# Optimization experiments

Hardware: AMD Instinct MI355X
Metric: run time of the kernel (lower is better)

## Reference

```python
import jax, jax.numpy as jnp
import numpy as np

N_NODES = 100000
N_EDGES = 1600000
IN_DIM = 128
OUT_DIM = 64


def setup_inputs() -> dict:
    key = jax.random.key(0)
    k1, k2, k3, k4, k5, k6 = jax.random.split(key, 6)
    x = jax.random.normal(k1, (N_NODES, IN_DIM), dtype=jnp.float32)
    edge_row = jax.random.randint(k2, (N_EDGES,), 0, N_NODES, dtype=jnp.int32)
    edge_col = jax.random.randint(k3, (N_EDGES,), 0, N_NODES, dtype=jnp.int32)
    edge_val = jax.random.uniform(k4, (N_EDGES,), dtype=jnp.float32)
    W = jax.random.normal(k5, (IN_DIM, OUT_DIM), dtype=jnp.float32) * (1.0 / np.sqrt(IN_DIM))
    b = jax.random.normal(k6, (OUT_DIM,), dtype=jnp.float32) * 0.01
    return {"x": x, "edge_row": edge_row, "edge_col": edge_col,
            "edge_val": edge_val, "W": W, "b": b}


def reference(x, edge_row, edge_col, edge_val, W, b):
    # xw = Linear(x)  -> [N, OUT_DIM]
    xw = x @ W + b
    # SpMM: (A_hat @ xw)[r] = sum_e val[e] * xw[col[e]] for edges with row[e]==r
    msgs = edge_val[:, None] * xw[edge_col]          # [E, OUT_DIM]
    ax = jax.ops.segment_sum(msgs, edge_row, num_segments=N_NODES)  # [N, OUT_DIM]
    # ReLU; dropout p=0.0 is identity (eval mode)
    return jax.nn.relu(ax)
```

## Files before the change

kernel.cpp:

```cpp
#include <hip/hip_runtime.h>
#include <hip/hip_fp16.h>
#include <limits.h>

#define IN_DIM 128
#define OUT_DIM 64
#define NBUCK 782
#define RPB 128
#define CHUNK 4096
#define SCAP 4096


typedef _Float16 half8_t __attribute__((ext_vector_type(8)));
typedef float    f32x4  __attribute__((ext_vector_type(4)));

__device__ __forceinline__ int kmap(int g, int j) {
    return g * 4 + (j & 3) + 16 * (j >> 2);
}

__global__ __launch_bounds__(256) void wfrag_kernel(
    const float* __restrict__ W, __half* __restrict__ wf) {
    for (int idx = threadIdx.x; idx < 4 * 4 * 64 * 8; idx += 256) {
        const int j    = idx & 7;
        const int lane = (idx >> 3) & 63;
        const int ks   = (idx >> 9) & 3;
        const int n    = idx >> 11;
        const int col  = n * 16 + (lane & 15);
        const int k    = ks * 32 + kmap(lane >> 4, j);
        wf[idx] = __float2half(W[k * OUT_DIM + col]);
    }
}

__global__ __launch_bounds__(256) void gemm_mfma_kernel(
    const float* __restrict__ x, const __half* __restrict__ wf,
    const float* __restrict__ b, __half* __restrict__ xw, int n_nodes) {
    const int t  = threadIdx.x;
    const int l  = t & 63;
    const int wv = t >> 6;
    const int g  = l >> 4;
    const int rowbase = blockIdx.x * 64 + wv * 16;
    const int row = rowbase + (l & 15);
    const bool rok = row < n_nodes;
    const float* xr = x + (size_t)row * IN_DIM;

    half8_t bf[4][4];
    const half8_t* wf8 = (const half8_t*)wf;
    #pragma unroll
    for (int n = 0; n < 4; ++n)
        #pragma unroll
        for (int ks = 0; ks < 4; ++ks)
            bf[n][ks] = wf8[(n * 4 + ks) * 64 + l];

    half8_t af[4];
    #pragma unroll
    for (int ks = 0; ks < 4; ++ks) {
        float4 c0 = rok ? *(const float4*)(xr + ks * 32 + g * 4)
                        : make_float4(0.f, 0.f, 0.f, 0.f);
        float4 c1 = rok ? *(const float4*)(xr + ks * 32 + 16 + g * 4)
                        : make_float4(0.f, 0.f, 0.f, 0.f);
        half8_t a;
        a[0] = (_Float16)c0.x; a[1] = (_Float16)c0.y;
        a[2] = (_Float16)c0.z; a[3] = (_Float16)c0.w;
        a[4] = (_Float16)c1.x; a[5] = (_Float16)c1.y;
        a[6] = (_Float16)c1.z; a[7] = (_Float16)c1.w;
        af[ks] = a;
    }

    f32x4 acc[4];
    #pragma unroll
    for (int n = 0; n < 4; ++n) acc[n] = (f32x4){0.f, 0.f, 0.f, 0.f};

    #pragma unroll
    for (int ks = 0; ks < 4; ++ks)
        #pragma unroll
        for (int n = 0; n < 4; ++n)
            acc[n] = __builtin_amdgcn_mfma_f32_16x16x32_f16(af[ks], bf[n][ks], acc[n], 0, 0, 0);

    float bias[4];
    #pragma unroll
    for (int n = 0; n < 4; ++n) bias[n] = b[n * 16 + (l & 15)];

    #pragma unroll
    for (int n = 0; n < 4; ++n)
        #pragma unroll
        for (int q = 0; q < 4; ++q) {
            const int ro = rowbase + g * 4 + q;
            if (ro < n_nodes)
                xw[(size_t)ro * OUT_DIM + n * 16 + (l & 15)] =
                    __float2half(acc[n][q] + bias[n]);
        }
}

__global__ __launch_bounds__(256) void bucket_hist_kernel(
    const int* __restrict__ erow, int* __restrict__ bcount, int n_edges) {
    __shared__ int h[NBUCK];
    for (int i = threadIdx.x; i < NBUCK; i += 256) h[i] = 0;
    __syncthreads();
    const int stride = gridDim.x * blockDim.x;
    for (int e = blockIdx.x * blockDim.x + threadIdx.x; e < n_edges; e += stride)
        atomicAdd(&h[erow[e] >> 7], 1);
    __syncthreads();
    for (int i = threadIdx.x; i < NBUCK; i += 256)
        if (h[i]) atomicAdd(&bcount[i], h[i]);
}

__global__ __launch_bounds__(512) void bucket_scan_kernel(
    const int* __restrict__ bcount, int* __restrict__ bbase,
    int* __restrict__ cursor, int* __restrict__ row_ptr, int n_nodes) {
    const int t = threadIdx.x;
    const int i0 = 2 * t, i1 = 2 * t + 1;
    int v0 = (i0 < NBUCK) ? bcount[i0] : 0;
    int v1 = (i1 < NBUCK) ? bcount[i1] : 0;
    const int s = v0 + v1;
    int inc = s;
    #pragma unroll
    for (int d = 1; d < 64; d <<= 1) {
        int u = __shfl_up(inc, d, 64);
        if ((t & 63) >= d) inc += u;
    }
    __shared__ int wsum[8];
    if ((t & 63) == 63) wsum[t >> 6] = inc;
    __syncthreads();
    int wp = 0;
    #pragma unroll
    for (int w = 0; w < 8; ++w) if (w < (t >> 6)) wp += wsum[w];
    const int ex = wp + (inc - s);
    if (i0 < NBUCK) { bbase[i0] = ex;      cursor[i0] = ex; }
    if (i1 < NBUCK) { bbase[i1] = ex + v0; cursor[i1] = ex + v0; }
    if (t == 511) {
        bbase[NBUCK] = wp + inc;
        row_ptr[n_nodes] = wp + inc;
    }
}

__global__ __launch_bounds__(512) void partition_kernel(
    const int* __restrict__ erow, const int* __restrict__ ecol,
    const float* __restrict__ eval_, int* __restrict__ cursor,
    int2* __restrict__ ecs, int n_edges) {
    __shared__ int  hist[NBUCK];
    __shared__ int  lbase[NBUCK];
    __shared__ int  gdelta[NBUCK];
    __shared__ int2 data[CHUNK];
    __shared__ int  gpos[CHUNK];
    __shared__ int  wsum[8];

    const int t = threadIdx.x;
    const int base = blockIdx.x * CHUNK;
    const int cnt = min(CHUNK, n_edges - base);

    for (int i = t; i < NBUCK; i += 512) hist[i] = 0;
    __syncthreads();

    int   myrow[CHUNK / 512];
    int   mycol[CHUNK / 512];
    float myval[CHUNK / 512];
    #pragma unroll
    for (int i = 0; i < CHUNK / 512; ++i) {
        const int idx = t + i * 512;
        if (idx < cnt) {
            const int e = base + idx;
            myrow[i] = erow[e];
            mycol[i] = ecol[e];
            myval[i] = eval_[e];
            atomicAdd(&hist[myrow[i] >> 7], 1);
        }
    }
    __syncthreads();

    {
        const int i0 = 2 * t, i1 = 2 * t + 1;
        const int v0 = (i0 < NBUCK) ? hist[i0] : 0;
        const int v1 = (i1 < NBUCK) ? hist[i1] : 0;
        const int s = v0 + v1;
        int inc = s;
        #pragma unroll
        for (int d = 1; d < 64; d <<= 1) {
            int u = __shfl_up(inc, d, 64);
            if ((t & 63) >= d) inc += u;
        }
        if ((t & 63) == 63) wsum[t >> 6] = inc;
        __syncthreads();
        int wp = 0;
        #pragma unroll
        for (int w = 0; w < 8; ++w) if (w < (t >> 6)) wp += wsum[w];
        const int ex = wp + (inc - s);
        if (i0 < NBUCK) lbase[i0] = ex;
        if (i1 < NBUCK) lbase[i1] = ex + v0;
    }
    __syncthreads();

    for (int i = t; i < NBUCK; i += 512) {
        const int c = hist[i];
        gdelta[i] = c ? (atomicAdd(&cursor[i], c) - lbase[i]) : 0;
    }
    __syncthreads();

    #pragma unroll
    for (int i = 0; i < CHUNK / 512; ++i) {
        const int idx = t + i * 512;
        if (idx < cnt) {
            const int bk = myrow[i] >> 7;
            const int slot = atomicAdd(&lbase[bk], 1);
            int2 p;
            p.x = (int)(((unsigned)(myrow[i] & (RPB - 1)) << 25) |
                        ((unsigned)mycol[i] << 7));
            p.y = __float_as_int(myval[i]);
            data[slot] = p;
            gpos[slot] = slot + gdelta[bk];
        }
    }
    __syncthreads();

    for (int slot = t; slot < cnt; slot += 512)
        ecs[gpos[slot]] = data[slot];
}

__global__ __launch_bounds__(256) void sort_bucket_kernel(
    const int* __restrict__ bbase, int2* __restrict__ ecs,
    int* __restrict__ row_ptr, int n_nodes) {
    __shared__ int2 data[SCAP];
    __shared__ int2 data2[SCAP];
    __shared__ int  hist[RPB];
    __shared__ int  wtot;

    const int bk = blockIdx.x;
    const int t  = threadIdx.x;
    const int s  = bbase[bk];
    const int e  = bbase[bk + 1];
    const int cnt = e - s;
    const int rbase = bk * RPB;

    if (cnt > SCAP) {
        for (int r = t; r < RPB; r += 256)
            if (rbase + r < n_nodes) row_ptr[rbase + r] = INT_MIN;
        return;
    }

    for (int i = t; i < RPB; i += 256) hist[i] = 0;
    __syncthreads();

    for (int i = t; i < cnt; i += 256) {
        const int2 p = ecs[s + i];
        data[i] = p;
        atomicAdd(&hist[((unsigned)p.x) >> 25], 1);
    }
    __syncthreads();

    int inc = 0, v = 0;
    if (t < RPB) {
        v = hist[t];
        inc = v;
        #pragma unroll
        for (int d = 1; d < 64; d <<= 1) {
            int u = __shfl_up(inc, d, 64);
            if ((t & 63) >= d) inc += u;
        }
        if (t == 63) wtot = inc;
    }
    __syncthreads();
    if (t < RPB) {
        if (t >= 64) inc += wtot;
        const int ex = inc - v;
        if (rbase + t < n_nodes) row_ptr[rbase + t] = s + ex;
        hist[t] = ex;
    }
    __syncthreads();

    for (int i = t; i < cnt; i += 256) {
        const int2 p = data[i];
        const int r = (int)(((unsigned)p.x) >> 25);
        const int pos = atomicAdd(&hist[r], 1);
        data2[pos] = p;
    }
    __syncthreads();

    for (int i = t; i < cnt; i += 256) ecs[s + i] = data2[i];
}

__global__ __launch_bounds__(256) void gather_relu_kernel(
    const __half* __restrict__ xw, const int2* __restrict__ ecs,
    const int* __restrict__ row_ptr, const int* __restrict__ bbase,
    float* __restrict__ out, int n_nodes, int n_edges) {
    const int lane = threadIdx.x & 63;
    const int q    = lane & 7;
    const int g    = lane >> 3;
    const int wid  = (blockIdx.x * blockDim.x + threadIdx.x) >> 6;
    const int r0   = wid * 2;
    const int r1   = r0 + 1;
    if (r0 >= n_nodes) return;
    const bool has1 = (r1 < n_nodes);
    const char* xwb = (const char*)xw;

    const int s0raw = row_ptr[r0];
    const int s1raw = has1 ? row_ptr[r1] : INT_MIN;
    const bool ok0 = (s0raw != INT_MIN);
    const bool ok1 = has1 && (s1raw != INT_MIN);

    float acc0[8], acc1[8];
    #pragma unroll
    for (int i = 0; i < 8; ++i) { acc0[i] = 0.f; acc1[i] = 0.f; }

    if (ok0 && (ok1 || !has1)) {
        int e0;
        {
            const int n0 = row_ptr[r0 + 1];
            e0 = (n0 == INT_MIN) ? bbase[(r0 >> 7) + 1] : n0;
        }
        int e1 = 0, j1 = 0;
        if (ok1) {
            const int n1 = row_ptr[r1 + 1];
            e1 = (n1 == INT_MIN) ? bbase[(r1 >> 7) + 1] : n1;
            j1 = s1raw;
        }
        int j0 = s0raw;

        while (j0 < e0 || j1 < e1) {
            const bool a0 = j0 < e0;
            const bool a1 = j1 < e1;
            int2 p0, p1; float v0 = 0.f, v1 = 0.f;
            unsigned off0 = 0, off1 = 0;
            if (a0) {
                const int ei = j0 + g;
                p0 = ecs[min(ei, n_edges - 1)];
                v0 = (ei < e0) ? __int_as_float(p0.y) : 0.f;
                off0 = (((unsigned)p0.x) & 0x01FFFF80u) | ((unsigned)q << 4);
            }
            if (a1) {
                const int ei = j1 + g;
                p1 = ecs[min(ei, n_edges - 1)];
                v1 = (ei < e1) ? __int_as_float(p1.y) : 0.f;
                off1 = (((unsigned)p1.x) & 0x01FFFF80u) | ((unsigned)q << 4);
            }
            union { uint4 u; __half2 h[4]; } U0, U1;
            if (a0) U0.u = *(const uint4*)(xwb + off0);
            if (a1) U1.u = *(const uint4*)(xwb + off1);
            if (a0) {
                #pragma unroll
                for (int i = 0; i < 4; ++i) {
                    const float2 f = __half22float2(U0.h[i]);
                    acc0[2 * i]     = fmaf(v0, f.x, acc0[2 * i]);
                    acc0[2 * i + 1] = fmaf(v0, f.y, acc0[2 * i + 1]);
                }
                j0 += 8;
            }
            if (a1) {
                #pragma unroll
                for (int i = 0; i < 4; ++i) {
                    const float2 f = __half22float2(U1.h[i]);
                    acc1[2 * i]     = fmaf(v1, f.x, acc1[2 * i]);
                    acc1[2 * i + 1] = fmaf(v1, f.y, acc1[2 * i + 1]);
                }
                j1 += 8;
            }
        }
    } else {
        #pragma unroll 1
        for (int rr = 0; rr < 2; ++rr) {
            const int r = r0 + rr;
            if (r >= n_nodes) break;
            float* acc = rr ? acc1 : acc0;
            const int sr = row_ptr[r];
            if (sr != INT_MIN) {
                int er;
                const int nr = row_ptr[r + 1];
                er = (nr == INT_MIN) ? bbase[(r >> 7) + 1] : nr;
                for (int j = sr; j < er; j += 8) {
                    const int ei = j + g;
                    const int2 p = ecs[min(ei, n_edges - 1)];
                    const float v = (ei < er) ? __int_as_float(p.y) : 0.f;
                    const unsigned off = (((unsigned)p.x) & 0x01FFFF80u) | ((unsigned)q << 4);
                    union { uint4 u; __half2 h[4]; } U;
                    U.u = *(const uint4*)(xwb + off);
                    #pragma unroll
                    for (int i = 0; i < 4; ++i) {
                        const float2 f = __half22float2(U.h[i]);
                        acc[2 * i]     = fmaf(v, f.x, acc[2 * i]);
                        acc[2 * i + 1] = fmaf(v, f.y, acc[2 * i + 1]);
                    }
                }
            } else {
                const int bk = r >> 7;
                const int bs = bbase[bk], be = bbase[bk + 1];
                const unsigned rl = (unsigned)(r & (RPB - 1));
                for (int j = bs; j < be; ++j) {
                    const int2 p = ecs[j];
                    if ((((unsigned)p.x) >> 25) == rl) {
                        const float v = __int_as_float(p.y);
                        const unsigned off = (((unsigned)p.x) & 0x01FFFF80u) | ((unsigned)q << 4);
                        union { uint4 u; __half2 h[4]; } U;
                        U.u = *(const uint4*)(xwb + off);
                        #pragma unroll
                        for (int i = 0; i < 4; ++i) {
                            const float2 f = __half22float2(U.h[i]);
                            acc[2 * i]     = fmaf(v * 0.125f, f.x, acc[2 * i]);
                            acc[2 * i + 1] = fmaf(v * 0.125f, f.y, acc[2 * i + 1]);
                        }
                    }
                }
                #pragma unroll
                for (int i = 0; i < 8; ++i) acc[i] *= 1.0f;
            }
        }
    }

    #pragma unroll
    for (int d = 8; d < 64; d <<= 1) {
        #pragma unroll
        for (int i = 0; i < 8; ++i) {
            acc0[i] += __shfl_xor(acc0[i], d, 64);
            acc1[i] += __shfl_xor(acc1[i], d, 64);
        }
    }

    if (g == 0) {
        {
            float4 o0, o1;
            o0.x = fmaxf(acc0[0], 0.f); o0.y = fmaxf(acc0[1], 0.f);
            o0.z = fmaxf(acc0[2], 0.f); o0.w = fmaxf(acc0[3], 0.f);
            o1.x = fmaxf(acc0[4], 0.f); o1.y = fmaxf(acc0[5], 0.f);
            o1.z = fmaxf(acc0[6], 0.f); o1.w = fmaxf(acc0[7], 0.f);
            float* op = out + (size_t)r0 * OUT_DIM + q * 8;
            *(float4*)(op)     = o0;
            *(float4*)(op + 4) = o1;
        }
        if (has1) {
            float4 o0, o1;
            o0.x = fmaxf(acc1[0], 0.f); o0.y = fmaxf(acc1[1], 0.f);
            o0.z = fmaxf(acc1[2], 0.f); o0.w = fmaxf(acc1[3], 0.f);
            o1.x = fmaxf(acc1[4], 0.f); o1.y = fmaxf(acc1[5], 0.f);
            o1.z = fmaxf(acc1[6], 0.f); o1.w = fmaxf(acc1[7], 0.f);
            float* op = out + (size_t)r1 * OUT_DIM + q * 8;
            *(float4*)(op)     = o0;
            *(float4*)(op + 4) = o1;
        }
    }
}

__global__ __launch_bounds__(256) void edge_scatter_kernel(
    const __half* __restrict__ xw, const int* __restrict__ erow,
    const int* __restrict__ ecol, const float* __restrict__ eval_,
    float* __restrict__ out, int n_edges) {
    const int lane  = threadIdx.x & 63;
    const int wid   = (blockIdx.x * blockDim.x + threadIdx.x) >> 6;
    const int nwave = (gridDim.x * blockDim.x) >> 6;
    for (int e = wid; e < n_edges; e += nwave) {
        const float m = eval_[e] * __half2float(xw[(size_t)ecol[e] * OUT_DIM + lane]);
        atomicAdd(&out[(size_t)erow[e] * OUT_DIM + lane], m);
    }
}

__global__ __launch_bounds__(256) void relu_kernel(float4* __restrict__ p, int n4) {
    const int stride = gridDim.x * blockDim.x;
    for (int i = blockIdx.x * blockDim.x + threadIdx.x; i < n4; i += stride) {
        float4 v = p[i];
        v.x = fmaxf(v.x, 0.f); v.y = fmaxf(v.y, 0.f);
        v.z = fmaxf(v.z, 0.f); v.w = fmaxf(v.w, 0.f);
        p[i] = v;
    }
}

extern "C" void kernel_launch(void* const* d_in, const int* in_sizes, int n_in,
                              void* d_out, int out_size, void* d_ws, size_t ws_size,
                              hipStream_t stream) {
    const float* x     = (const float*)d_in[0];
    const int*   erow  = (const int*)d_in[1];
    const int*   ecol  = (const int*)d_in[2];
    const float* eval_ = (const float*)d_in[3];
    const float* W     = (const float*)d_in[4];
    const float* b     = (const float*)d_in[5];
    float*       out   = (float*)d_out;

    const int n_nodes = in_sizes[0] / IN_DIM;
    const int n_edges = in_sizes[1];

    auto align256 = [](size_t v) { return (v + 255) & ~(size_t)255; };
    size_t off_xw     = 0;
    size_t off_wf     = align256(off_xw     + (size_t)n_nodes * OUT_DIM * 2);
    size_t off_bcount = align256(off_wf     + (size_t)4 * 4 * 64 * 8 * 2);
    size_t off_bbase  = align256(off_bcount + (size_t)NBUCK * 4);
    size_t off_cursor = align256(off_bbase  + (size_t)(NBUCK + 1) * 4);
    size_t off_rowptr = align256(off_cursor + (size_t)NBUCK * 4);
    size_t off_ecs    = align256(off_rowptr + (size_t)(n_nodes + 1) * 4);
    size_t need       = off_ecs + (size_t)n_edges * 8;

    __half* xw = (__half*)((char*)d_ws + off_xw);
    __half* wf = (__half*)((char*)d_ws + off_wf);

    wfrag_kernel<<<1, 256, 0, stream>>>(W, wf);
    gemm_mfma_kernel<<<(n_nodes + 63) / 64, 256, 0, stream>>>(x, wf, b, xw, n_nodes);

    if (need <= ws_size && n_nodes <= NBUCK * RPB && n_edges > 0) {
        int*  bcount = (int*)((char*)d_ws + off_bcount);
        int*  bbase  = (int*)((char*)d_ws + off_bbase);
        int*  cursor = (int*)((char*)d_ws + off_cursor);
        int*  rowptr = (int*)((char*)d_ws + off_rowptr);
        int2* ecs    = (int2*)((char*)d_ws + off_ecs);

        hipMemsetAsync(bcount, 0, (size_t)NBUCK * 4, stream);
        bucket_hist_kernel<<<512, 256, 0, stream>>>(erow, bcount, n_edges);
        bucket_scan_kernel<<<1, 512, 0, stream>>>(bcount, bbase, cursor, rowptr, n_nodes);
        partition_kernel<<<(n_edges + CHUNK - 1) / CHUNK, 512, 0, stream>>>(
            erow, ecol, eval_, cursor, ecs, n_edges);
        sort_bucket_kernel<<<NBUCK, 256, 0, stream>>>(bbase, ecs, rowptr, n_nodes);
        gather_relu_kernel<<<(n_nodes + 7) / 8, 256, 0, stream>>>(
            xw, ecs, rowptr, bbase, out, n_nodes, n_edges);
    } else {
        hipMemsetAsync(d_out, 0, (size_t)out_size * sizeof(float), stream);
        edge_scatter_kernel<<<8192, 256, 0, stream>>>(xw, erow, ecol, eval_, out, n_edges);
        relu_kernel<<<2048, 256, 0, stream>>>((float4*)d_out, out_size / 4);
    }
}
```

Measured before the change: 121.6 us.

## Fuse bucket histogram into GEMM, drop scan kernel and memset, use nontemporal loads

Moves the bucket histogram into the GEMM kernel and folds the W-fragment prep, counter zeroing and row_ptr end into one prep kernel, which removes the memset and the separate histogram launch. The global bucket scan is recomputed redundantly in each partition and sort block, so the single-block scan kernel goes away. The sort kernel now scatters straight back to global memory instead of through a second shared buffer, and edge streams use nontemporal loads. The aim is fewer launches and serialisation points, at the cost of redundant scans per block and uncoalesced scatter writes in the sort.

```diff
diff --git a/kernel.cpp b/kernel.cpp
--- a/kernel.cpp
+++ b/kernel.cpp
@@ -13,13 +13,24 @@
 typedef _Float16 half8_t __attribute__((ext_vector_type(8)));
 typedef float    f32x4  __attribute__((ext_vector_type(4)));
 
+__device__ __forceinline__ int2 ldnt2(const int2* p) {
+    const long long v = __builtin_nontemporal_load((const long long*)p);
+    int2 r;
+    r.x = (int)(unsigned)((unsigned long long)v & 0xffffffffull);
+    r.y = (int)(unsigned)((unsigned long long)v >> 32);
+    return r;
+}
+
 __device__ __forceinline__ int kmap(int g, int j) {
     return g * 4 + (j & 3) + 16 * (j >> 2);
 }
 
-__global__ __launch_bounds__(256) void wfrag_kernel(
-    const float* __restrict__ W, __half* __restrict__ wf) {
-    for (int idx = threadIdx.x; idx < 4 * 4 * 64 * 8; idx += 256) {
+__global__ __launch_bounds__(256) void prep_kernel(
+    const float* __restrict__ W, __half* __restrict__ wf,
+    int* __restrict__ bcount, int* __restrict__ cursor,
+    int* __restrict__ row_ptr, int n_nodes, int n_edges) {
+    const int t = threadIdx.x;
+    for (int idx = t; idx < 4 * 4 * 64 * 8; idx += 256) {
         const int j    = idx & 7;
         const int lane = (idx >> 3) & 63;
         const int ks   = (idx >> 9) & 3;
@@ -28,11 +39,16 @@
         const int k    = ks * 32 + kmap(lane >> 4, j);
         wf[idx] = __float2half(W[k * OUT_DIM + col]);
     }
-}
-
-__global__ __launch_bounds__(256) void gemm_mfma_kernel(
+    if (bcount)
+        for (int i = t; i < NBUCK; i += 256) { bcount[i] = 0; cursor[i] = 0; }
+    if (row_ptr && t == 0) row_ptr[n_nodes] = n_edges;
+}
+
+__global__ __launch_bounds__(256) void gemm_hist_kernel(
     const float* __restrict__ x, const __half* __restrict__ wf,
-    const float* __restrict__ b, __half* __restrict__ xw, int n_nodes) {
+    const float* __restrict__ b, __half* __restrict__ xw, int n_nodes,
+    const int* __restrict__ erow, int* __restrict__ bcount, int n_edges) {
+    __shared__ int h[NBUCK];
     const int t  = threadIdx.x;
     const int l  = t & 63;
     const int wv = t >> 6;
@@ -88,57 +104,29 @@
                 xw[(size_t)ro * OUT_DIM + n * 16 + (l & 15)] =
                     __float2half(acc[n][q] + bias[n]);
         }
-}
-
-__global__ __launch_bounds__(256) void bucket_hist_kernel(
-    const int* __restrict__ erow, int* __restrict__ bcount, int n_edges) {
-    __shared__ int h[NBUCK];
-    for (int i = threadIdx.x; i < NBUCK; i += 256) h[i] = 0;
-    __syncthreads();
-    const int stride = gridDim.x * blockDim.x;
-    for (int e = blockIdx.x * blockDim.x + threadIdx.x; e < n_edges; e += stride)
-        atomicAdd(&h[erow[e] >> 7], 1);
-    __syncthreads();
-    for (int i = threadIdx.x; i < NBUCK; i += 256)
-        if (h[i]) atomicAdd(&bcount[i], h[i]);
-}
-
-__global__ __launch_bounds__(512) void bucket_scan_kernel(
-    const int* __restrict__ bcount, int* __restrict__ bbase,
-    int* __restrict__ cursor, int* __restrict__ row_ptr, int n_nodes) {
-    const int t = threadIdx.x;
-    const int i0 = 2 * t, i1 = 2 * t + 1;
-    int v0 = (i0 < NBUCK) ? bcount[i0] : 0;
-    int v1 = (i1 < NBUCK) ? bcount[i1] : 0;
-    const int s = v0 + v1;
-    int inc = s;
-    #pragma unroll
-    for (int d = 1; d < 64; d <<= 1) {
-        int u = __shfl_up(inc, d, 64);
-        if ((t & 63) >= d) inc += u;
-    }
-    __shared__ int wsum[8];
-    if ((t & 63) == 63) wsum[t >> 6] = inc;
-    __syncthreads();
-    int wp = 0;
-    #pragma unroll
-    for (int w = 0; w < 8; ++w) if (w < (t >> 6)) wp += wsum[w];
-    const int ex = wp + (inc - s);
-    if (i0 < NBUCK) { bbase[i0] = ex;      cursor[i0] = ex; }
-    if (i1 < NBUCK) { bbase[i1] = ex + v0; cursor[i1] = ex + v0; }
-    if (t == 511) {
-        bbase[NBUCK] = wp + inc;
-        row_ptr[n_nodes] = wp + inc;
+
+    if (bcount) {
+        for (int i = t; i < NBUCK; i += 256) h[i] = 0;
+        __syncthreads();
+        if (blockIdx.x < 512) {
+            const int stride = 512 * 256;
+            for (int e = blockIdx.x * 256 + t; e < n_edges; e += stride)
+                atomicAdd(&h[__builtin_nontemporal_load(&erow[e]) >> 7], 1);
+        }
+        __syncthreads();
+        for (int i = t; i < NBUCK; i += 256)
+            if (h[i]) atomicAdd(&bcount[i], h[i]);
     }
 }
 
 __global__ __launch_bounds__(512) void partition_kernel(
     const int* __restrict__ erow, const int* __restrict__ ecol,
-    const float* __restrict__ eval_, int* __restrict__ cursor,
-    int2* __restrict__ ecs, int n_edges) {
+    const float* __restrict__ eval_, const int* __restrict__ bcount,
+    int* __restrict__ cursor, int2* __restrict__ ecs, int n_edges) {
     __shared__ int  hist[NBUCK];
     __shared__ int  lbase[NBUCK];
     __shared__ int  gdelta[NBUCK];
+    __shared__ int  sbase[NBUCK];
     __shared__ int2 data[CHUNK];
     __shared__ int  gpos[CHUNK];
     __shared__ int  wsum[8];
@@ -148,7 +136,27 @@
     const int cnt = min(CHUNK, n_edges - base);
 
     for (int i = t; i < NBUCK; i += 512) hist[i] = 0;
-    __syncthreads();
+
+    {
+        const int i0 = 2 * t, i1 = 2 * t + 1;
+        const int v0 = (i0 < NBUCK) ? bcount[i0] : 0;
+        const int v1 = (i1 < NBUCK) ? bcount[i1] : 0;
+        const int s2 = v0 + v1;
+        int inc = s2;
+        #pragma unroll
+        for (int d = 1; d < 64; d <<= 1) {
+            int u = __shfl_up(inc, d, 64);
+            if ((t & 63) >= d) inc += u;
+        }
+        if ((t & 63) == 63) wsum[t >> 6] = inc;
+        __syncthreads();
+        int wp = 0;
+        #pragma unroll
+        for (int w = 0; w < 8; ++w) if (w < (t >> 6)) wp += wsum[w];
+        const int ex = wp + (inc - s2);
+        if (i0 < NBUCK) sbase[i0] = ex;
+        if (i1 < NBUCK) sbase[i1] = ex + v0;
+    }
 
     int   myrow[CHUNK / 512];
     int   mycol[CHUNK / 512];
@@ -158,9 +166,9 @@
         const int idx = t + i * 512;
         if (idx < cnt) {
             const int e = base + idx;
-            myrow[i] = erow[e];
-            mycol[i] = ecol[e];
-            myval[i] = eval_[e];
+            myrow[i] = __builtin_nontemporal_load(&erow[e]);
+            mycol[i] = __builtin_nontemporal_load(&ecol[e]);
+            myval[i] = __builtin_nontemporal_load(&eval_[e]);
             atomicAdd(&hist[myrow[i] >> 7], 1);
         }
     }
@@ -170,8 +178,8 @@
         const int i0 = 2 * t, i1 = 2 * t + 1;
         const int v0 = (i0 < NBUCK) ? hist[i0] : 0;
         const int v1 = (i1 < NBUCK) ? hist[i1] : 0;
-        const int s = v0 + v1;
-        int inc = s;
+        const int s2 = v0 + v1;
+        int inc = s2;
         #pragma unroll
         for (int d = 1; d < 64; d <<= 1) {
             int u = __shfl_up(inc, d, 64);
@@ -182,7 +190,7 @@
         int wp = 0;
         #pragma unroll
         for (int w = 0; w < 8; ++w) if (w < (t >> 6)) wp += wsum[w];
-        const int ex = wp + (inc - s);
+        const int ex = wp + (inc - s2);
         if (i0 < NBUCK) lbase[i0] = ex;
         if (i1 < NBUCK) lbase[i1] = ex + v0;
     }
@@ -190,7 +198,7 @@
 
     for (int i = t; i < NBUCK; i += 512) {
         const int c = hist[i];
-        gdelta[i] = c ? (atomicAdd(&cursor[i], c) - lbase[i]) : 0;
+        gdelta[i] = c ? (sbase[i] + atomicAdd(&cursor[i], c) - lbase[i]) : 0;
     }
     __syncthreads();
 
@@ -214,32 +222,61 @@
         ecs[gpos[slot]] = data[slot];
 }
 
-__global__ __launch_bounds__(256) void sort_bucket_kernel(
-    const int* __restrict__ bbase, int2* __restrict__ ecs,
-    int* __restrict__ row_ptr, int n_nodes) {
+__global__ __launch_bounds__(512) void sort_kernel(
+    const int* __restrict__ bcount, int2* __restrict__ ecs,
+    int* __restrict__ row_ptr, int* __restrict__ bbase, int n_nodes) {
     __shared__ int2 data[SCAP];
-    __shared__ int2 data2[SCAP];
     __shared__ int  hist[RPB];
+    __shared__ int  sbase[NBUCK + 1];
+    __shared__ int  wsum[8];
     __shared__ int  wtot;
 
     const int bk = blockIdx.x;
     const int t  = threadIdx.x;
-    const int s  = bbase[bk];
-    const int e  = bbase[bk + 1];
+
+    if (t < RPB) hist[t] = 0;
+
+    {
+        const int i0 = 2 * t, i1 = 2 * t + 1;
+        const int v0 = (i0 < NBUCK) ? bcount[i0] : 0;
+        const int v1 = (i1 < NBUCK) ? bcount[i1] : 0;
+        const int s2 = v0 + v1;
+        int inc = s2;
+        #pragma unroll
+        for (int d = 1; d < 64; d <<= 1) {
+            int u = __shfl_up(inc, d, 64);
+            if ((t & 63) >= d) inc += u;
+        }
+        if ((t & 63) == 63) wsum[t >> 6] = inc;
+        __syncthreads();
+        int wp = 0;
+        #pragma unroll
+        for (int w = 0; w < 8; ++w) if (w < (t >> 6)) wp += wsum[w];
+        const int ex = wp + (inc - s2);
+        if (i0 < NBUCK) sbase[i0] = ex;
+        if (i1 < NBUCK) sbase[i1] = ex + v0;
+        if (t == 511) sbase[NBUCK] = wp + inc;
+    }
+    __syncthreads();
+
+    const int s   = sbase[bk];
+    const int e   = sbase[bk + 1];
     const int cnt = e - s;
     const int rbase = bk * RPB;
 
+    if (t == 0) {
+        bbase[bk] = s;
+        if (bk == NBUCK - 1 || bk == gridDim.x - 1) bbase[bk + 1] = e;
+    }
+
     if (cnt > SCAP) {
-        for (int r = t; r < RPB; r += 256)
+        for (int r = t; r < RPB; r += 512)
             if (rbase + r < n_nodes) row_ptr[rbase + r] = INT_MIN;
         return;
     }
 
-    for (int i = t; i < RPB; i += 256) hist[i] = 0;
-    __syncthreads();
-
-    for (int i = t; i < cnt; i += 256) {
-        const int2 p = ecs[s + i];
+    for (int i = t; i < cnt; i += 512) {
+        const int2 p = ldnt2(&ecs[s + i]);
         data[i] = p;
         atomicAdd(&hist[((unsigned)p.x) >> 25], 1);
     }
@@ -265,15 +302,11 @@
     }
     __syncthreads();
 
-    for (int i = t; i < cnt; i += 256) {
+    for (int i = t; i < cnt; i += 512) {
         const int2 p = data[i];
-        const int r = (int)(((unsigned)p.x) >> 25);
-        const int pos = atomicAdd(&hist[r], 1);
-        data2[pos] = p;
-    }
-    __syncthreads();
-
-    for (int i = t; i < cnt; i += 256) ecs[s + i] = data2[i];
+        const int pos = atomicAdd(&hist[((unsigned)p.x) >> 25], 1);
+        ecs[s + pos] = p;
+    }
 }
 
 __global__ __launch_bounds__(256) void gather_relu_kernel(
@@ -320,13 +353,13 @@
             unsigned off0 = 0, off1 = 0;
             if (a0) {
                 const int ei = j0 + g;
-                p0 = ecs[min(ei, n_edges - 1)];
+                p0 = ldnt2(&ecs[min(ei, n_edges - 1)]);
                 v0 = (ei < e0) ? __int_as_float(p0.y) : 0.f;
                 off0 = (((unsigned)p0.x) & 0x01FFFF80u) | ((unsigned)q << 4);
             }
             if (a1) {
                 const int ei = j1 + g;
-                p1 = ecs[min(ei, n_edges - 1)];
+                p1 = ldnt2(&ecs[min(ei, n_edges - 1)]);
                 v1 = (ei < e1) ? __int_as_float(p1.y) : 0.f;
                 off1 = (((unsigned)p1.x) & 0x01FFFF80u) | ((unsigned)q << 4);
             }
@@ -360,12 +393,11 @@
             float* acc = rr ? acc1 : acc0;
             const int sr = row_ptr[r];
             if (sr != INT_MIN) {
-                int er;
                 const int nr = row_ptr[r + 1];
-                er = (nr == INT_MIN) ? bbase[(r >> 7) + 1] : nr;
+                const int er = (nr == INT_MIN) ? bbase[(r >> 7) + 1] : nr;
                 for (int j = sr; j < er; j += 8) {
                     const int ei = j + g;
-                    const int2 p = ecs[min(ei, n_edges - 1)];
+                    const int2 p = ldnt2(&ecs[min(ei, n_edges - 1)]);
                     const float v = (ei < er) ? __int_as_float(p.y) : 0.f;
                     const unsigned off = (((unsigned)p.x) & 0x01FFFF80u) | ((unsigned)q << 4);
                     union { uint4 u; __half2 h[4]; } U;
@@ -382,7 +414,7 @@
                 const int bs = bbase[bk], be = bbase[bk + 1];
                 const unsigned rl = (unsigned)(r & (RPB - 1));
                 for (int j = bs; j < be; ++j) {
-                    const int2 p = ecs[j];
+                    const int2 p = ldnt2(&ecs[j]);
                     if ((((unsigned)p.x) >> 25) == rl) {
                         const float v = __int_as_float(p.y);
                         const unsigned off = (((unsigned)p.x) & 0x01FFFF80u) | ((unsigned)q << 4);
@@ -396,8 +428,6 @@
                         }
                     }
                 }
-                #pragma unroll
-                for (int i = 0; i < 8; ++i) acc[i] *= 1.0f;
             }
         }
     }
@@ -476,34 +506,36 @@
     size_t off_xw     = 0;
     size_t off_wf     = align256(off_xw     + (size_t)n_nodes * OUT_DIM * 2);
     size_t off_bcount = align256(off_wf     + (size_t)4 * 4 * 64 * 8 * 2);
-    size_t off_bbase  = align256(off_bcount + (size_t)NBUCK * 4);
-    size_t off_cursor = align256(off_bbase  + (size_t)(NBUCK + 1) * 4);
-    size_t off_rowptr = align256(off_cursor + (size_t)NBUCK * 4);
+    size_t off_cursor = align256(off_bcount + (size_t)NBUCK * 4);
+    size_t off_bbase  = align256(off_cursor + (size_t)NBUCK * 4);
+    size_t off_rowptr = align256(off_bbase  + (size_t)(NBUCK + 1) * 4);
     size_t off_ecs    = align256(off_rowptr + (size_t)(n_nodes + 1) * 4);
     size_t need       = off_ecs + (size_t)n_edges * 8;
 
     __half* xw = (__half*)((char*)d_ws + off_xw);
     __half* wf = (__half*)((char*)d_ws + off_wf);
 
-    wfrag_kernel<<<1, 256, 0, stream>>>(W, wf);
-    gemm_mfma_kernel<<<(n_nodes + 63) / 64, 256, 0, stream>>>(x, wf, b, xw, n_nodes);
-
-    if (need <= ws_size && n_nodes <= NBUCK * RPB && n_edges > 0) {
+    const bool main_path = (need <= ws_size) && (n_nodes <= NBUCK * RPB) && (n_edges > 0);
+
+    if (main_path) {
         int*  bcount = (int*)((char*)d_ws + off_bcount);
+        int*  cursor = (int*)((char*)d_ws + off_cursor);
         int*  bbase  = (int*)((char*)d_ws + off_bbase);
-        int*  cursor = (int*)((char*)d_ws + off_cursor);
         int*  rowptr = (int*)((char*)d_ws + off_rowptr);
         int2* ecs    = (int2*)((char*)d_ws + off_ecs);
 
-        hipMemsetAsync(bcount, 0, (size_t)NBUCK * 4, stream);
-        bucket_hist_kernel<<<512, 256, 0, stream>>>(erow, bcount, n_edges);
-        bucket_scan_kernel<<<1, 512, 0, stream>>>(bcount, bbase, cursor, rowptr, n_nodes);
+        prep_kernel<<<1, 256, 0, stream>>>(W, wf, bcount, cursor, rowptr, n_nodes, n_edges);
+        gemm_hist_kernel<<<(n_nodes + 63) / 64, 256, 0, stream>>>(
+            x, wf, b, xw, n_nodes, erow, bcount, n_edges);
         partition_kernel<<<(n_edges + CHUNK - 1) / CHUNK, 512, 0, stream>>>(
-            erow, ecol, eval_, cursor, ecs, n_edges);
-        sort_bucket_kernel<<<NBUCK, 256, 0, stream>>>(bbase, ecs, rowptr, n_nodes);
+            erow, ecol, eval_, bcount, cursor, ecs, n_edges);
+        sort_kernel<<<NBUCK, 512, 0, stream>>>(bcount, ecs, rowptr, bbase, n_nodes);
         gather_relu_kernel<<<(n_nodes + 7) / 8, 256, 0, stream>>>(
             xw, ecs, rowptr, bbase, out, n_nodes, n_edges);
     } else {
+        prep_kernel<<<1, 256, 0, stream>>>(W, wf, nullptr, nullptr, nullptr, n_nodes, n_edges);
+        gemm_hist_kernel<<<(n_nodes + 63) / 64, 256, 0, stream>>>(
+            x, wf, b, xw, n_nodes, nullptr, nullptr, 0);
         hipMemsetAsync(d_out, 0, (size_t)out_size * sizeof(float), stream);
         edge_scatter_kernel<<<8192, 256, 0, stream>>>(xw, erow, ecol, eval_, out, n_edges);
         relu_kernel<<<2048, 256, 0, stream>>>((float4*)d_out, out_size / 4);
```

Measured after the change: 128.3 us. 1.06x slower.
